# Kernel tuning notes

Measured on AMD Instinct MI355X. Metric: run time of the kernel, lower is better.

Reference implementation:

```python
import jax, jax.numpy as jnp
import numpy as np

INPUT_DIM = 2048
HIDDEN_DIM = 256  # max(input_dim // 8, 32)
NUM_EXPERTS = 16
TOP_K = 2
Z_LOSS_COEF = 0.005
LB_COEF = 0.005
LN_EPS = 1e-5


def setup_inputs() -> dict:
    key = jax.random.key(0)
    k1, k2, k3 = jax.random.split(key, 3)
    B, S = 4, 4096
    x = jax.random.normal(k1, (B, S, INPUT_DIM), dtype=jnp.float32)
    # orthogonal-ish init approximated by scaled gaussian (math is identical regardless of values)
    Wp = jax.random.normal(k2, (HIDDEN_DIM, INPUT_DIM), dtype=jnp.float32) * (0.3 / np.sqrt(INPUT_DIM))
    Wg = jax.random.normal(k3, (NUM_EXPERTS, HIDDEN_DIM), dtype=jnp.float32) * (0.3 / np.sqrt(HIDDEN_DIM))
    ln_w = jnp.ones((HIDDEN_DIM,), dtype=jnp.float32)
    ln_b = jnp.zeros((HIDDEN_DIM,), dtype=jnp.float32)
    temperature = jnp.ones((1,), dtype=jnp.float32) * 0.07
    return {"x": x, "Wp": Wp, "Wg": Wg, "ln_w": ln_w, "ln_b": ln_b, "temperature": temperature}


def reference(x, Wp, Wg, ln_w, ln_b, temperature):
    B, S, D = x.shape
    xr = x.reshape(-1, D)                                  # [T, D]
    proj = jnp.einsum('td,hd->th', xr, Wp)                 # [T, H]
    mu = proj.mean(-1, keepdims=True)
    var = jnp.mean(jnp.square(proj - mu), axis=-1, keepdims=True)
    normalized = (proj - mu) * jax.lax.rsqrt(var + LN_EPS) * ln_w + ln_b
    logits = jnp.einsum('th,eh->te', normalized, Wg)       # [T, E]
    # temperature used via .item() in torch -> constant w.r.t. autodiff
    temp = jax.lax.stop_gradient(jnp.abs(temperature) + 1e-6)[0]
    logits = logits / temp
    routing_weights = jax.nn.softmax(logits, axis=-1)      # [T, E]
    top_k_w, top_k_i = jax.lax.top_k(routing_weights, TOP_K)
    top_k_w = top_k_w / (top_k_w.sum(-1, keepdims=True) + 1e-6)
    T = routing_weights.shape[0]
    dispatch = jnp.zeros_like(routing_weights).at[jnp.arange(T)[:, None], top_k_i].set(top_k_w)
    # load-balance KL: F.kl_div(actual.log(), ideal, reduction='batchmean')
    E = routing_weights.shape[-1]
    actual_load = routing_weights.mean(0)                  # [E]
    ideal = 1.0 / E
    load_balance_loss = jnp.sum(ideal * (jnp.log(ideal) - jnp.log(actual_load))) / E
    router_z_loss = jnp.mean(jnp.square(logits))
    router_loss = Z_LOSS_COEF * router_z_loss + LB_COEF * load_balance_loss
    return (jax.lax.stop_gradient(routing_weights), dispatch.reshape(B, S, E), router_loss)
```

## Files before the change

kernel.cpp:

```cpp
#include <hip/hip_runtime.h>
#include <hip/hip_bf16.h>
#include <math.h>

#define D 2048
#define H 256
#define E 16
#define TMB 32
#define BK 16
#define NCH (D / BK)
#define LDK 20
#define LDXK 16
#define WP_OFF 0
#define X_OFF  5120
#define SB_LDW 260
#define SB_OFF 0
#define WG_OFF 8320
#define LB_OFF 12416
#define Z_OFF  12432
#define SMEM_FLOATS 12448
#define THREADS 512
#define WS_STRIDE 20

__global__ __launch_bounds__(THREADS)
void router_main(const float* __restrict__ x, const float* __restrict__ Wp,
                 const float* __restrict__ Wg, const float* __restrict__ lnw_g,
                 const float* __restrict__ lnb_g, const float* __restrict__ temp_g,
                 float* __restrict__ out_rw, float* __restrict__ out_disp,
                 float* __restrict__ ws_part)
{
    __shared__ __align__(16) float smem[SMEM_FLOATS];
    const int t  = threadIdx.x;
    const int tx = t & 15;
    const int ku = (t >> 4) & 3;
    const int tb = (t >> 6) & 3;
    const int hb = t >> 8;
    const int tok0 = blockIdx.x * TMB;

    float acc[8][8];
    #pragma unroll
    for (int i = 0; i < 8; ++i)
        #pragma unroll
        for (int j = 0; j < 8; ++j) acc[i][j] = 0.f;

    const int wrow = t >> 1;
    const int wcol = (t & 1) * 8;
    const int xrw  = t >> 2;
    const int xcl  = (t & 3) * 4;
    float4 wpr0, wpr1, xr;
    auto ISSUE = [&](int k0) {
        wpr0 = *(const float4*)&Wp[(size_t)wrow * D + k0 + wcol];
        wpr1 = *(const float4*)&Wp[(size_t)wrow * D + k0 + wcol + 4];
        if (t < 128) xr = *(const float4*)&x[(size_t)(tok0 + xrw) * D + k0 + xcl];
    };
    ISSUE(0);

    const float* wbase = &smem[WP_OFF + (hb * 128 + tx) * LDK + ku * 4];
    const float* xbase = &smem[X_OFF + (tb * 8) * LDXK + ku * 4];

    for (int c = 0; c < NCH; ++c) {
        __syncthreads();
        *(float4*)&smem[WP_OFF + wrow * LDK + wcol]     = wpr0;
        *(float4*)&smem[WP_OFF + wrow * LDK + wcol + 4] = wpr1;
        if (t < 128) *(float4*)&smem[X_OFF + xrw * LDXK + xcl] = xr;
        __syncthreads();
        if (c + 1 < NCH) ISSUE((c + 1) * BK);

        float4 xa[8];
        #pragma unroll
        for (int i = 0; i < 8; ++i)
            xa[i] = *(const float4*)&xbase[i * LDXK];
        #pragma unroll
        for (int j = 0; j < 8; ++j) {
            const float4 wv = *(const float4*)&wbase[j * 16 * LDK];
            #pragma unroll
            for (int i = 0; i < 8; ++i) {
                acc[i][j] = fmaf(xa[i].x, wv.x, acc[i][j]);
                acc[i][j] = fmaf(xa[i].y, wv.y, acc[i][j]);
                acc[i][j] = fmaf(xa[i].z, wv.z, acc[i][j]);
                acc[i][j] = fmaf(xa[i].w, wv.w, acc[i][j]);
            }
        }
    }

    #pragma unroll
    for (int i = 0; i < 8; ++i)
        #pragma unroll
        for (int j = 0; j < 8; ++j) {
            acc[i][j] += __shfl_xor(acc[i][j], 16);
            acc[i][j] += __shfl_xor(acc[i][j], 32);
        }

    __syncthreads();

    if (ku == 0) {
        #pragma unroll
        for (int i = 0; i < 8; ++i)
            #pragma unroll
            for (int j = 0; j < 8; ++j)
                smem[SB_OFF + (tb * 8 + i) * SB_LDW + hb * 128 + tx + 16 * j] = acc[i][j];
    }
    {
        const int fi = t * 8;
        *(float4*)&smem[WG_OFF + fi]     = *(const float4*)&Wg[fi];
        *(float4*)&smem[WG_OFF + fi + 4] = *(const float4*)&Wg[fi + 4];
    }
    if (t < 16)  smem[LB_OFF + t] = 0.f;
    if (t == 16) smem[Z_OFF] = 0.f;
    __syncthreads();

    const int ptx  = t & 15;
    const int tokl = t >> 4;
    const int tok  = tok0 + tokl;

    float pr[16];
    #pragma unroll
    for (int j = 0; j < 16; ++j)
        pr[j] = smem[SB_OFF + tokl * SB_LDW + ptx + 16 * j];

    float lnw[16], lnb[16];
    #pragma unroll
    for (int j = 0; j < 16; ++j) {
        lnw[j] = lnw_g[ptx + 16 * j];
        lnb[j] = lnb_g[ptx + 16 * j];
    }
    const float temp = fabsf(temp_g[0]) + 1e-6f;

    float s = 0.f;
    #pragma unroll
    for (int j = 0; j < 16; ++j) s += pr[j];
    s += __shfl_xor(s, 1); s += __shfl_xor(s, 2);
    s += __shfl_xor(s, 4); s += __shfl_xor(s, 8);
    const float mu = s * (1.f / 256.f);
    float v = 0.f;
    #pragma unroll
    for (int j = 0; j < 16; ++j) { const float d = pr[j] - mu; v = fmaf(d, d, v); }
    v += __shfl_xor(v, 1); v += __shfl_xor(v, 2);
    v += __shfl_xor(v, 4); v += __shfl_xor(v, 8);
    const float rstd = 1.0f / sqrtf(v * (1.f / 256.f) + 1e-5f);

    float n[16];
    #pragma unroll
    for (int j = 0; j < 16; ++j)
        n[j] = fmaf((pr[j] - mu) * rstd, lnw[j], lnb[j]);

    float p[16];
    #pragma unroll
    for (int e = 0; e < 16; ++e) p[e] = 0.f;
    #pragma unroll
    for (int j = 0; j < 16; ++j) {
        const float nv = n[j];
        const int  h   = ptx + 16 * j;
        #pragma unroll
        for (int e = 0; e < 16; ++e)
            p[e] = fmaf(nv, smem[WG_OFF + e * H + h], p[e]);
    }
    #pragma unroll
    for (int m = 1; m < 16; m <<= 1)
        #pragma unroll
        for (int e = 0; e < 16; ++e) p[e] += __shfl_xor(p[e], m);
    #pragma unroll
    for (int e = 0; e < 16; ++e) p[e] = p[e] / temp;

    float myz = 0.f;
    if (ptx == 0) {
        #pragma unroll
        for (int e = 0; e < 16; ++e) myz = fmaf(p[e], p[e], myz);
    }

    float mx = p[0];
    #pragma unroll
    for (int e = 1; e < 16; ++e) mx = fmaxf(mx, p[e]);
    float w[16]; float sw = 0.f;
    #pragma unroll
    for (int e = 0; e < 16; ++e) { w[e] = expf(p[e] - mx); sw += w[e]; }
    #pragma unroll
    for (int e = 0; e < 16; ++e) w[e] = w[e] / sw;

    float w1 = -1.f; int i1 = 0; float w2 = -1.f; int i2 = 0;
    #pragma unroll
    for (int e = 0; e < 16; ++e) {
        const float we = w[e];
        if (we > w1)      { w2 = w1; i2 = i1; w1 = we; i1 = e; }
        else if (we > w2) { w2 = we; i2 = e; }
    }
    const float rs = 1.f / (w1 + w2 + 1e-6f);
    out_rw  [(size_t)tok * E + ptx] = w[ptx];
    out_disp[(size_t)tok * E + ptx] = (ptx == i1) ? w1 * rs : (ptx == i2 ? w2 * rs : 0.f);

    atomicAdd(&smem[LB_OFF + ptx], w[ptx]);
    if (ptx == 0) atomicAdd(&smem[Z_OFF], myz);
    __syncthreads();
    if (t < 16)  ws_part[blockIdx.x * WS_STRIDE + t]  = smem[LB_OFF + t];
    if (t == 16) ws_part[blockIdx.x * WS_STRIDE + 16] = smem[Z_OFF];
}

__global__ void router_final(const float* __restrict__ ws_part,
                             float* __restrict__ out_loss, int nblocks, int T)
{
    const int l = threadIdx.x;
    float lb[16]; float z = 0.f;
    #pragma unroll
    for (int e = 0; e < 16; ++e) lb[e] = 0.f;
    for (int b = l; b < nblocks; b += 64) {
        #pragma unroll
        for (int e = 0; e < 16; ++e) lb[e] += ws_part[b * WS_STRIDE + e];
        z += ws_part[b * WS_STRIDE + 16];
    }
    #pragma unroll
    for (int m = 1; m < 64; m <<= 1) {
        #pragma unroll
        for (int e = 0; e < 16; ++e) lb[e] += __shfl_xor(lb[e], m);
        z += __shfl_xor(z, m);
    }
    if (l == 0) {
        const float zloss = z / (float)(T * 16);
        const float ideal = 1.f / 16.f;
        float lbl = 0.f;
        #pragma unroll
        for (int e = 0; e < 16; ++e) {
            const float a = lb[e] / (float)T;
            lbl += ideal * (logf(ideal) - logf(a));
        }
        lbl *= (1.f / 16.f);
        out_loss[0] = 0.005f * zloss + 0.005f * lbl;
    }
}

extern "C" void kernel_launch(void* const* d_in, const int* in_sizes, int n_in,
                              void* d_out, int out_size, void* d_ws, size_t ws_size,
                              hipStream_t stream)
{
    const float* x    = (const float*)d_in[0];
    const float* Wp   = (const float*)d_in[1];
    const float* Wg   = (const float*)d_in[2];
    const float* lnw  = (const float*)d_in[3];
    const float* lnb  = (const float*)d_in[4];
    const float* temp = (const float*)d_in[5];
    const int T = in_sizes[0] / D;
    float* out      = (float*)d_out;
    float* out_rw   = out;
    float* out_disp = out + (size_t)T * E;
    float* out_loss = out + (size_t)2 * T * E;
    float* ws_part  = (float*)d_ws;
    const int nblocks = T / TMB;

    hipLaunchKernelGGL(router_main, dim3(nblocks), dim3(THREADS), 0, stream,
                       x, Wp, Wg, lnw, lnb, temp, out_rw, out_disp, ws_part);
    hipLaunchKernelGGL(router_final, dim3(1), dim3(64), 0, stream,
                       ws_part, out_loss, nblocks, T);
}
```

Measured before the change: 300.5 us.

## Double token tile per block to 64 and use 1024 threads with two-pass epilogue

Each block now computes 64 tokens with 1024 threads, so every Wp chunk staged in shared memory feeds twice as many tokens. This roughly halves Wp re-reads from L2 across the grid. The LayerNorm, gating and softmax epilogue runs in two passes of 32 tokens so the shared scratch stays the same size. Load-balance partial sums are reduced with wave shuffles before the shared atomics, which cuts atomic traffic. The cost is half as many blocks (one per CU) and higher register pressure under the new launch bounds.

```diff
diff --git a/kernel.cpp b/kernel.cpp
--- a/kernel.cpp
+++ b/kernel.cpp
@@ -5,23 +5,22 @@
 #define D 2048
 #define H 256
 #define E 16
-#define TMB 32
+#define TMB 64
 #define BK 16
 #define NCH (D / BK)
 #define LDK 20
-#define LDXK 16
 #define WP_OFF 0
-#define X_OFF  5120
-#define SB_LDW 260
+#define X_OFF 5120
+#define SB_LDW 257
 #define SB_OFF 0
-#define WG_OFF 8320
-#define LB_OFF 12416
-#define Z_OFF  12432
-#define SMEM_FLOATS 12448
-#define THREADS 512
+#define WG_OFF 8224
+#define LB_OFF 12320
+#define Z_OFF  12336
+#define SMEM_FLOATS 12352
+#define THREADS 1024
 #define WS_STRIDE 20
 
-__global__ __launch_bounds__(THREADS)
+__global__ __launch_bounds__(THREADS, 4)
 void router_main(const float* __restrict__ x, const float* __restrict__ Wp,
                  const float* __restrict__ Wg, const float* __restrict__ lnw_g,
                  const float* __restrict__ lnb_g, const float* __restrict__ temp_g,
@@ -32,52 +31,51 @@
     const int t  = threadIdx.x;
     const int tx = t & 15;
     const int ku = (t >> 4) & 3;
-    const int tb = (t >> 6) & 3;
-    const int hb = t >> 8;
+    const int wv = t >> 6;
+    const int tb = wv & 7;
+    const int hb = wv >> 3;
+    const int wrow = t >> 2;
+    const int wcol = (t & 3) << 2;
     const int tok0 = blockIdx.x * TMB;
 
+    *(float4*)&smem[WG_OFF + 4 * t] = *(const float4*)&Wg[4 * t];
+
     float acc[8][8];
     #pragma unroll
     for (int i = 0; i < 8; ++i)
         #pragma unroll
         for (int j = 0; j < 8; ++j) acc[i][j] = 0.f;
 
-    const int wrow = t >> 1;
-    const int wcol = (t & 1) * 8;
-    const int xrw  = t >> 2;
-    const int xcl  = (t & 3) * 4;
-    float4 wpr0, wpr1, xr;
+    float4 wpr, xr;
     auto ISSUE = [&](int k0) {
-        wpr0 = *(const float4*)&Wp[(size_t)wrow * D + k0 + wcol];
-        wpr1 = *(const float4*)&Wp[(size_t)wrow * D + k0 + wcol + 4];
-        if (t < 128) xr = *(const float4*)&x[(size_t)(tok0 + xrw) * D + k0 + xcl];
+        wpr = *(const float4*)&Wp[(size_t)wrow * D + k0 + wcol];
+        if (t < 256) xr = *(const float4*)&x[(size_t)(tok0 + wrow) * D + k0 + wcol];
     };
     ISSUE(0);
 
     const float* wbase = &smem[WP_OFF + (hb * 128 + tx) * LDK + ku * 4];
-    const float* xbase = &smem[X_OFF + (tb * 8) * LDXK + ku * 4];
+    const float* xbase = &smem[X_OFF + tb * 128 + ku * 4];
 
     for (int c = 0; c < NCH; ++c) {
         __syncthreads();
-        *(float4*)&smem[WP_OFF + wrow * LDK + wcol]     = wpr0;
-        *(float4*)&smem[WP_OFF + wrow * LDK + wcol + 4] = wpr1;
-        if (t < 128) *(float4*)&smem[X_OFF + xrw * LDXK + xcl] = xr;
+        *(float4*)&smem[WP_OFF + wrow * LDK + wcol] = wpr;
+        if (t < 256) *(float4*)&smem[X_OFF + wrow * 16 + wcol] = xr;
         __syncthreads();
         if (c + 1 < NCH) ISSUE((c + 1) * BK);
 
         float4 xa[8];
         #pragma unroll
         for (int i = 0; i < 8; ++i)
-            xa[i] = *(const float4*)&xbase[i * LDXK];
+            xa[i] = *(const float4*)&xbase[i * 16];
         #pragma unroll
         for (int j = 0; j < 8; ++j) {
-            const float4 wv = *(const float4*)&wbase[j * 16 * LDK];
+            const float4 wvv = *(const float4*)&wbase[j * 16 * LDK];
             #pragma unroll
             for (int i = 0; i < 8; ++i) {
-                acc[i][j] = fmaf(xa[i].x, wv.x, acc[i][j]);
-                acc[i][j] = fmaf(xa[i].y, wv.y, acc[i][j]);
-                acc[i][j] = fmaf(xa[i].z, wv.z, acc[i][j]);
-                acc[i][j] = fmaf(xa[i].w, wv.w, acc[i][j]);
+                acc[i][j] = fmaf(xa[i].x, wvv.x, acc[i][j]);
+                acc[i][j] = fmaf(xa[i].y, wvv.y, acc[i][j]);
+                acc[i][j] = fmaf(xa[i].z, wvv.z, acc[i][j]);
+                acc[i][j] = fmaf(xa[i].w, wvv.w, acc[i][j]);
             }
         }
     }
@@ -92,103 +90,114 @@
 
     __syncthreads();
 
-    if (ku == 0) {
-        #pragma unroll
-        for (int i = 0; i < 8; ++i)
-            #pragma unroll
-            for (int j = 0; j < 8; ++j)
-                smem[SB_OFF + (tb * 8 + i) * SB_LDW + hb * 128 + tx + 16 * j] = acc[i][j];
-    }
-    {
-        const int fi = t * 8;
-        *(float4*)&smem[WG_OFF + fi]     = *(const float4*)&Wg[fi];
-        *(float4*)&smem[WG_OFF + fi + 4] = *(const float4*)&Wg[fi + 4];
-    }
-    if (t < 16)  smem[LB_OFF + t] = 0.f;
-    if (t == 16) smem[Z_OFF] = 0.f;
-    __syncthreads();
-
-    const int ptx  = t & 15;
-    const int tokl = t >> 4;
-    const int tok  = tok0 + tokl;
-
-    float pr[16];
-    #pragma unroll
-    for (int j = 0; j < 16; ++j)
-        pr[j] = smem[SB_OFF + tokl * SB_LDW + ptx + 16 * j];
-
+    const float temp = fabsf(temp_g[0]) + 1e-6f;
     float lnw[16], lnb[16];
-    #pragma unroll
-    for (int j = 0; j < 16; ++j) {
-        lnw[j] = lnw_g[ptx + 16 * j];
-        lnb[j] = lnb_g[ptx + 16 * j];
-    }
-    const float temp = fabsf(temp_g[0]) + 1e-6f;
-
-    float s = 0.f;
-    #pragma unroll
-    for (int j = 0; j < 16; ++j) s += pr[j];
-    s += __shfl_xor(s, 1); s += __shfl_xor(s, 2);
-    s += __shfl_xor(s, 4); s += __shfl_xor(s, 8);
-    const float mu = s * (1.f / 256.f);
-    float v = 0.f;
-    #pragma unroll
-    for (int j = 0; j < 16; ++j) { const float d = pr[j] - mu; v = fmaf(d, d, v); }
-    v += __shfl_xor(v, 1); v += __shfl_xor(v, 2);
-    v += __shfl_xor(v, 4); v += __shfl_xor(v, 8);
-    const float rstd = 1.0f / sqrtf(v * (1.f / 256.f) + 1e-5f);
-
-    float n[16];
-    #pragma unroll
-    for (int j = 0; j < 16; ++j)
-        n[j] = fmaf((pr[j] - mu) * rstd, lnw[j], lnb[j]);
-
-    float p[16];
-    #pragma unroll
-    for (int e = 0; e < 16; ++e) p[e] = 0.f;
-    #pragma unroll
-    for (int j = 0; j < 16; ++j) {
-        const float nv = n[j];
-        const int  h   = ptx + 16 * j;
-        #pragma unroll
-        for (int e = 0; e < 16; ++e)
-            p[e] = fmaf(nv, smem[WG_OFF + e * H + h], p[e]);
-    }
-    #pragma unroll
-    for (int m = 1; m < 16; m <<= 1)
-        #pragma unroll
-        for (int e = 0; e < 16; ++e) p[e] += __shfl_xor(p[e], m);
-    #pragma unroll
-    for (int e = 0; e < 16; ++e) p[e] = p[e] / temp;
-
-    float myz = 0.f;
-    if (ptx == 0) {
-        #pragma unroll
-        for (int e = 0; e < 16; ++e) myz = fmaf(p[e], p[e], myz);
-    }
-
-    float mx = p[0];
-    #pragma unroll
-    for (int e = 1; e < 16; ++e) mx = fmaxf(mx, p[e]);
-    float w[16]; float sw = 0.f;
-    #pragma unroll
-    for (int e = 0; e < 16; ++e) { w[e] = expf(p[e] - mx); sw += w[e]; }
-    #pragma unroll
-    for (int e = 0; e < 16; ++e) w[e] = w[e] / sw;
-
-    float w1 = -1.f; int i1 = 0; float w2 = -1.f; int i2 = 0;
-    #pragma unroll
-    for (int e = 0; e < 16; ++e) {
-        const float we = w[e];
-        if (we > w1)      { w2 = w1; i2 = i1; w1 = we; i1 = e; }
-        else if (we > w2) { w2 = we; i2 = e; }
-    }
-    const float rs = 1.f / (w1 + w2 + 1e-6f);
-    out_rw  [(size_t)tok * E + ptx] = w[ptx];
-    out_disp[(size_t)tok * E + ptx] = (ptx == i1) ? w1 * rs : (ptx == i2 ? w2 * rs : 0.f);
-
-    atomicAdd(&smem[LB_OFF + ptx], w[ptx]);
-    if (ptx == 0) atomicAdd(&smem[Z_OFF], myz);
+    if (t < 512) {
+        #pragma unroll
+        for (int j = 0; j < 16; ++j) {
+            lnw[j] = lnw_g[(t & 15) + 16 * j];
+            lnb[j] = lnb_g[(t & 15) + 16 * j];
+        }
+    }
+    float mylb = 0.f, myz = 0.f;
+
+    #pragma unroll
+    for (int pass = 0; pass < 2; ++pass) {
+        if (ku == 0 && (tb >> 2) == pass) {
+            const int rb = (tb & 3) * 8;
+            #pragma unroll
+            for (int i = 0; i < 8; ++i)
+                #pragma unroll
+                for (int j = 0; j < 8; ++j)
+                    smem[SB_OFF + (rb + i) * SB_LDW + hb * 128 + tx + 16 * j] = acc[i][j];
+        }
+        if (pass == 0) {
+            if (t < 16)  smem[LB_OFF + t] = 0.f;
+            if (t == 16) smem[Z_OFF] = 0.f;
+        }
+        __syncthreads();
+
+        if (t < 512) {
+            const int ptx  = t & 15;
+            const int tokl = t >> 4;
+            const int tok  = tok0 + pass * 32 + tokl;
+
+            float pr[16];
+            #pragma unroll
+            for (int j = 0; j < 16; ++j)
+                pr[j] = smem[SB_OFF + tokl * SB_LDW + ptx + 16 * j];
+
+            float s = 0.f;
+            #pragma unroll
+            for (int j = 0; j < 16; ++j) s += pr[j];
+            s += __shfl_xor(s, 1); s += __shfl_xor(s, 2);
+            s += __shfl_xor(s, 4); s += __shfl_xor(s, 8);
+            const float mu = s * (1.f / 256.f);
+            float v = 0.f;
+            #pragma unroll
+            for (int j = 0; j < 16; ++j) { const float d = pr[j] - mu; v = fmaf(d, d, v); }
+            v += __shfl_xor(v, 1); v += __shfl_xor(v, 2);
+            v += __shfl_xor(v, 4); v += __shfl_xor(v, 8);
+            const float rstd = 1.0f / sqrtf(v * (1.f / 256.f) + 1e-5f);
+
+            float n[16];
+            #pragma unroll
+            for (int j = 0; j < 16; ++j)
+                n[j] = fmaf((pr[j] - mu) * rstd, lnw[j], lnb[j]);
+
+            float p[16];
+            #pragma unroll
+            for (int e = 0; e < 16; ++e) p[e] = 0.f;
+            #pragma unroll
+            for (int j = 0; j < 16; ++j) {
+                const float nv = n[j];
+                const int  h   = ptx + 16 * j;
+                #pragma unroll
+                for (int e = 0; e < 16; ++e)
+                    p[e] = fmaf(nv, smem[WG_OFF + e * H + h], p[e]);
+            }
+            #pragma unroll
+            for (int m = 1; m < 16; m <<= 1)
+                #pragma unroll
+                for (int e = 0; e < 16; ++e) p[e] += __shfl_xor(p[e], m);
+            #pragma unroll
+            for (int e = 0; e < 16; ++e) p[e] = p[e] / temp;
+
+            if (ptx == 0) {
+                #pragma unroll
+                for (int e = 0; e < 16; ++e) myz = fmaf(p[e], p[e], myz);
+            }
+
+            float mx = p[0];
+            #pragma unroll
+            for (int e = 1; e < 16; ++e) mx = fmaxf(mx, p[e]);
+            float w[16]; float sw = 0.f;
+            #pragma unroll
+            for (int e = 0; e < 16; ++e) { w[e] = expf(p[e] - mx); sw += w[e]; }
+            #pragma unroll
+            for (int e = 0; e < 16; ++e) w[e] = w[e] / sw;
+            mylb += w[ptx];
+
+            float w1 = -1.f; int i1 = 0; float w2 = -1.f; int i2 = 0;
+            #pragma unroll
+            for (int e = 0; e < 16; ++e) {
+                const float we = w[e];
+                if (we > w1)      { w2 = w1; i2 = i1; w1 = we; i1 = e; }
+                else if (we > w2) { w2 = we; i2 = e; }
+            }
+            const float rs = 1.f / (w1 + w2 + 1e-6f);
+            out_rw  [(size_t)tok * E + ptx] = w[ptx];
+            out_disp[(size_t)tok * E + ptx] = (ptx == i1) ? w1 * rs : (ptx == i2 ? w2 * rs : 0.f);
+        }
+        __syncthreads();
+    }
+
+    if (t < 512) {
+        mylb += __shfl_xor(mylb, 16); mylb += __shfl_xor(mylb, 32);
+        myz  += __shfl_xor(myz, 16);  myz  += __shfl_xor(myz, 32);
+        if ((t & 63) < 16) atomicAdd(&smem[LB_OFF + (t & 15)], mylb);
+        if ((t & 63) == 0) atomicAdd(&smem[Z_OFF], myz);
+    }
     __syncthreads();
     if (t < 16)  ws_part[blockIdx.x * WS_STRIDE + t]  = smem[LB_OFF + t];
     if (t == 16) ws_part[blockIdx.x * WS_STRIDE + 16] = smem[Z_OFF];
```

After: 294.9 us. Within noise of the previous version (-1.9%).
